# Kernel optimization log

Measured on AMD Instinct MI355X. Metric: run time of the kernel, lower is better.

## Reference

```python
import jax, jax.numpy as jnp
import numpy as np

B, N, D_IN, D, H = 4, 256, 600, 600, 256  # batch, nodes, in_dim, mem_dim, attn hidden


def setup_inputs() -> dict:
    key = jax.random.key(0)
    ks = jax.random.split(key, 12)
    feature = jax.random.normal(ks[0], (B, N, D_IN), dtype=jnp.float32)
    latent_adj = jax.random.randint(ks[1], (B, N, N), 0, 2).astype(jnp.float32)
    s_in = 1.0 / np.sqrt(D_IN)
    s_d = 1.0 / np.sqrt(D)
    s_2d = 1.0 / np.sqrt(2 * D)
    s_h = 1.0 / np.sqrt(H)
    W0 = jax.random.uniform(ks[2], (D_IN, D), jnp.float32, -s_in, s_in)
    b0 = jax.random.uniform(ks[3], (D,), jnp.float32, -s_in, s_in)
    W1 = jax.random.uniform(ks[4], (D, D), jnp.float32, -s_d, s_d)
    b1 = jax.random.uniform(ks[5], (D,), jnp.float32, -s_d, s_d)
    aW1 = jax.random.uniform(ks[6], (2 * D, H), jnp.float32, -s_2d, s_2d)
    ab1 = jax.random.uniform(ks[7], (H,), jnp.float32, -s_2d, s_2d)
    aW2 = jax.random.uniform(ks[8], (H,), jnp.float32, -s_h, s_h)
    ab2 = jax.random.uniform(ks[9], (1,), jnp.float32, -s_h, s_h)
    return {"feature": feature, "latent_adj": latent_adj, "W0": W0, "b0": b0,
            "W1": W1, "b1": b1, "aW1": aW1, "ab1": ab1, "aW2": aW2, "ab2": ab2}


def _gat_layer(x, Wl, bl, aW1, ab1, aW2, ab2, adj):
    h = jnp.einsum('bni,io->bno', x, Wl) + bl                    # [B,N,D]
    # Decompose first attn linear: [h_i, h_j] @ aW1 = h_i @ aW1[:D] + h_j @ aW1[D:]
    left = jnp.einsum('bnd,dh->bnh', h, aW1[:h.shape[-1]])        # i-part
    right = jnp.einsum('bnd,dh->bnh', h, aW1[h.shape[-1]:])       # j-part
    hid = jax.nn.relu(left[:, :, None, :] + right[:, None, :, :] + ab1)  # [B,N,N,H]
    e = jax.nn.leaky_relu(jnp.einsum('bijh,h->bij', hid, aW2) + ab2[0],
                          negative_slope=0.01)                    # [B,N,N]
    e = jnp.where(adj == 0, jnp.float32(-1e9), e)
    attention = jax.nn.softmax(e, axis=-1) * adj
    return jax.nn.relu(jnp.einsum('bij,bjd->bid', attention, h))


def reference(feature, latent_adj, W0, b0, W1, b1, aW1, ab1, aW2, ab2):
    h = _gat_layer(feature, W0, b0, aW1, ab1, aW2, ab2, latent_adj)
    h = _gat_layer(h, W1, b1, aW1, ab1, aW2, ab2, latent_adj)
    return h
```

## Files before the change

### kernel.cpp

```cpp
#include <hip/hip_runtime.h>
#include <hip/hip_bf16.h>

#define BATCH 4
#define NN    256
#define DD    600
#define HH    256
#define MROWS (BATCH*NN)
#define KPAD  640

typedef __attribute__((ext_vector_type(8))) short bf16x8;
typedef __attribute__((ext_vector_type(4))) float f32x4;

__device__ __forceinline__ void gload16(const void* g, void* l)
{
    __builtin_amdgcn_global_load_lds(
        (const __attribute__((address_space(1))) void*)g,
        (__attribute__((address_space(3))) void*)l, 16, 0, 0);
}

__device__ __forceinline__ void waitcnt_vm(int n)
{
    switch (n) {
    case 0:  asm volatile("s_waitcnt vmcnt(0)"  ::: "memory"); break;
    case 4:  asm volatile("s_waitcnt vmcnt(4)"  ::: "memory"); break;
    case 8:  asm volatile("s_waitcnt vmcnt(8)"  ::: "memory"); break;
    case 12: asm volatile("s_waitcnt vmcnt(12)" ::: "memory"); break;
    default: asm volatile("s_waitcnt vmcnt(0)"  ::: "memory"); break;
    }
}

template<bool BIAS, bool RELU, bool WF32, bool WB16, bool WHT, int NK>
__global__ __launch_bounds__(256) void gemm_mfma(
    const __hip_bfloat16* __restrict__ A, const __hip_bfloat16* __restrict__ BT,
    const float* __restrict__ bias,
    float* __restrict__ Cf, __hip_bfloat16* __restrict__ Cb,
    __hip_bfloat16* __restrict__ hT,
    int lda, int ldb, int ldcf, int ldcb, int Nvalid, int biasN,
    long long sA, long long sBT, long long sCf, long long sCb)
{
    __shared__ __align__(16) char lds[65536];

    const int bz   = blockIdx.z;
    const int tid  = threadIdx.x;
    const int lane = tid & 63;
    const int wid  = tid >> 6;
    const int wr   = wid >> 1;
    const int wc   = wid & 1;
    const int row0 = blockIdx.y * 64;
    const int col0 = blockIdx.x * 64;

    const char* Ab = (const char*)A + (bz * sA + (long long)row0 * lda) * 2;
    const char* Bb = (const char*)BT + (bz * sBT + (long long)col0 * ldb) * 2;

    const int sr   = tid >> 3;
    const int scb  = (tid & 7) * 16;
    const int scbs = scb ^ ((sr & 7) << 4);

    const char* gA0 = Ab + (long long)sr        * (lda * 2) + scbs;
    const char* gA1 = Ab + (long long)(sr + 32) * (lda * 2) + scbs;
    const char* gB0 = Bb + (long long)sr        * (ldb * 2) + scbs;
    const char* gB1 = Bb + (long long)(sr + 32) * (ldb * 2) + scbs;

    f32x4 acc[2][2] = {};

    const int fr = lane & 15;
    const int kg = (lane >> 4) * 16;
    const int xv = (fr & 7) << 4;

    auto issue = [&](int t) {
        char* bA = lds + (t & 3) * 8192;
        char* bB = lds + 32768 + (t & 3) * 8192;
        const long long off = (long long)t * 128;
        gload16(gA0 + off, bA + wid * 1024);
        gload16(gA1 + off, bA + 4096 + wid * 1024);
        gload16(gB0 + off, bB + wid * 1024);
        gload16(gB1 + off, bB + 4096 + wid * 1024);
    };

    constexpr int PRE = (NK < 3) ? NK : 3;
    #pragma unroll
    for (int p = 0; p < PRE; ++p) issue(p);

    #pragma unroll
    for (int t = 0; t < NK; ++t) {
        const int imax = (t + 2 < NK - 1) ? t + 2 : NK - 1;
        waitcnt_vm(4 * (imax - t));
        __builtin_amdgcn_s_barrier();
        const char* ldsA = lds + (t & 3) * 8192;
        const char* ldsB = lds + 32768 + (t & 3) * 8192;
        #pragma unroll
        for (int ks = 0; ks < 2; ++ks) {
            const int kb = ks * 64 + kg;
            bf16x8 a0 = *(const bf16x8*)(ldsA + (wr * 32 + fr)      * 128 + (kb ^ xv));
            bf16x8 a1 = *(const bf16x8*)(ldsA + (wr * 32 + 16 + fr) * 128 + (kb ^ xv));
            bf16x8 b0 = *(const bf16x8*)(ldsB + (wc * 32 + fr)      * 128 + (kb ^ xv));
            bf16x8 b1 = *(const bf16x8*)(ldsB + (wc * 32 + 16 + fr) * 128 + (kb ^ xv));
            acc[0][0] = __builtin_amdgcn_mfma_f32_16x16x32_bf16(a0, b0, acc[0][0], 0, 0, 0);
            acc[0][1] = __builtin_amdgcn_mfma_f32_16x16x32_bf16(a0, b1, acc[0][1], 0, 0, 0);
            acc[1][0] = __builtin_amdgcn_mfma_f32_16x16x32_bf16(a1, b0, acc[1][0], 0, 0, 0);
            acc[1][1] = __builtin_amdgcn_mfma_f32_16x16x32_bf16(a1, b1, acc[1][1], 0, 0, 0);
        }
        if (t + 3 < NK) issue(t + 3);
    }
    __syncthreads();

    const int er = (lane >> 4) * 4;
    const int ec = lane & 15;
    __hip_bfloat16* sT = (__hip_bfloat16*)lds;

    #pragma unroll
    for (int mi = 0; mi < 2; ++mi) {
        #pragma unroll
        for (int ni = 0; ni < 2; ++ni) {
            const int lr0 = wr * 32 + mi * 16 + er;
            const int lc  = wc * 32 + ni * 16 + ec;
            const int gr = row0 + lr0;
            const int gc = col0 + lc;
            const float bv = (BIAS && gc < biasN) ? bias[gc] : 0.f;
            #pragma unroll
            for (int r = 0; r < 4; ++r) {
                float v = acc[mi][ni][r] + bv;
                if (RELU) v = fmaxf(v, 0.f);
                const __hip_bfloat16 hv = __float2bfloat16(v);
                const long long row = gr + r;
                if (WF32 && gc < Nvalid)
                    Cf[bz * sCf + row * ldcf + gc] = v;
                if (WB16)
                    Cb[bz * sCb + row * ldcb + gc] = hv;
                if (WHT)
                    sT[(lr0 + r) * 72 + lc] = hv;
            }
        }
    }

    if (WHT) {
        __syncthreads();
        const int b  = row0 >> 8;
        const int i0 = row0 & 255;
        const int cc = tid >> 3;
        const int ch = tid & 7;
        #pragma unroll
        for (int p = 0; p < 2; ++p) {
            const int d = col0 + cc + p * 32;
            __align__(16) __hip_bfloat16 tmp[8];
            #pragma unroll
            for (int u = 0; u < 8; ++u)
                tmp[u] = sT[(ch * 8 + u) * 72 + cc + p * 32];
            *(float4*)&hT[((long long)b * KPAD + d) * NN + i0 + ch * 8] = *(float4*)tmp;
        }
    }
}

__global__ __launch_bounds__(256) void prep_kernel(
    const float* __restrict__ feature, const float* __restrict__ W0,
    const float* __restrict__ W1, const float* __restrict__ aW1,
    __hip_bfloat16* __restrict__ xb, __hip_bfloat16* __restrict__ W0T,
    __hip_bfloat16* __restrict__ W1T, __hip_bfloat16* __restrict__ aW1T)
{
    const int bid = blockIdx.x;
    const int tid = threadIdx.x;
    if (bid < 640) {
        const int idx = (bid * 256 + tid) * 4;
        const int r = idx / KPAD, c = idx % KPAD;
        float4 v = make_float4(0.f, 0.f, 0.f, 0.f);
        if (c < DD) v = *(const float4*)&feature[r * DD + c];
        __align__(8) __hip_bfloat16 o[4] = {
            __float2bfloat16(v.x), __float2bfloat16(v.y),
            __float2bfloat16(v.z), __float2bfloat16(v.w)};
        *(float2*)&xb[idx] = *(float2*)o;
        return;
    }
    __shared__ float tile[32][33];
    const int t = bid - 640;
    const int which = (t < 400) ? 0 : (t < 800) ? 1 : 2;
    const int tt = (which == 0) ? t : (which == 1) ? t - 400 : t - 800;
    const int n0 = (tt / 20) * 32;
    const int k0 = (tt % 20) * 32;
    const int tx = tid & 31, ty = tid >> 5;
    #pragma unroll
    for (int r = 0; r < 4; ++r) {
        const int k = k0 + ty + r * 8;
        const int n = n0 + tx;
        float v = 0.f;
        if (which == 0)      { if (k < DD && n < DD) v = W0[k * DD + n]; }
        else if (which == 1) { if (k < DD && n < DD) v = W1[k * DD + n]; }
        else                 { if (k < DD) v = (n < HH) ? aW1[k * HH + n]
                                                        : aW1[(DD + k) * HH + (n - HH)]; }
        tile[ty + r * 8][tx] = v;
    }
    __syncthreads();
    __hip_bfloat16* dst = (which == 0) ? W0T : (which == 1) ? W1T : aW1T;
    #pragma unroll
    for (int r = 0; r < 4; ++r) {
        const int n = n0 + ty + r * 8;
        const int k = k0 + tx;
        dst[n * KPAD + k] = __float2bfloat16(tile[tx][ty + r * 8]);
    }
}

__device__ __forceinline__ void block_max4(float* v, float (*red)[4])
{
    #pragma unroll
    for (int o = 32; o > 0; o >>= 1)
        #pragma unroll
        for (int q = 0; q < 4; ++q) v[q] = fmaxf(v[q], __shfl_down(v[q], o));
    const int lane = threadIdx.x & 63, w = threadIdx.x >> 6;
    if (lane == 0) { red[w][0]=v[0]; red[w][1]=v[1]; red[w][2]=v[2]; red[w][3]=v[3]; }
    __syncthreads();
    #pragma unroll
    for (int q = 0; q < 4; ++q)
        v[q] = fmaxf(fmaxf(red[0][q], red[1][q]), fmaxf(red[2][q], red[3][q]));
    __syncthreads();
}

__device__ __forceinline__ void block_sum4(float* v, float (*red)[4])
{
    #pragma unroll
    for (int o = 32; o > 0; o >>= 1)
        #pragma unroll
        for (int q = 0; q < 4; ++q) v[q] += __shfl_down(v[q], o);
    const int lane = threadIdx.x & 63, w = threadIdx.x >> 6;
    if (lane == 0) { red[w][0]=v[0]; red[w][1]=v[1]; red[w][2]=v[2]; red[w][3]=v[3]; }
    __syncthreads();
    #pragma unroll
    for (int q = 0; q < 4; ++q)
        v[q] = red[0][q] + red[1][q] + red[2][q] + red[3][q];
    __syncthreads();
}

__global__ __launch_bounds__(256) void attn_kernel(
    const float* __restrict__ LR, const float* __restrict__ aW2,
    const float* __restrict__ ab2, const float* __restrict__ adj,
    __hip_bfloat16* __restrict__ att)
{
    __shared__ float sL[4][HH];
    __shared__ float sW[HH];
    __shared__ float red[4][4];

    const int b  = blockIdx.y;
    const int i0 = blockIdx.x * 4;
    const int j  = threadIdx.x;

    sW[j] = aW2[j];
    #pragma unroll
    for (int q = 0; q < 4; ++q)
        sL[q][j] = LR[((long long)(b * NN + i0 + q)) * 512 + j];
    __syncthreads();

    const float* rp = LR + ((long long)(b * NN + j)) * 512 + HH;
    float acc[4] = {0.f, 0.f, 0.f, 0.f};
    for (int h = 0; h < HH; h += 8) {
        const float4 ra = *(const float4*)(rp + h);
        const float4 rb = *(const float4*)(rp + h + 4);
        const float4 w0 = *(const float4*)&sW[h];
        const float4 w1 = *(const float4*)&sW[h + 4];
        #pragma unroll
        for (int q = 0; q < 4; ++q) {
            const float4 l0 = *(const float4*)&sL[q][h];
            const float4 l1 = *(const float4*)&sL[q][h + 4];
            float s = fmaxf(l0.x + ra.x, 0.f) * w0.x;
            s += fmaxf(l0.y + ra.y, 0.f) * w0.y;
            s += fmaxf(l0.z + ra.z, 0.f) * w0.z;
            s += fmaxf(l0.w + ra.w, 0.f) * w0.w;
            s += fmaxf(l1.x + rb.x, 0.f) * w1.x;
            s += fmaxf(l1.y + rb.y, 0.f) * w1.y;
            s += fmaxf(l1.z + rb.z, 0.f) * w1.z;
            s += fmaxf(l1.w + rb.w, 0.f) * w1.w;
            acc[q] += s;
        }
    }

    const float ab2v = ab2[0];
    float m[4], a[4];
    #pragma unroll
    for (int q = 0; q < 4; ++q) {
        float e = acc[q] + ab2v;
        e = (e > 0.f) ? e : 0.01f * e;
        a[q] = adj[((long long)(b * NN + i0 + q)) * NN + j];
        m[q] = (a[q] == 0.f) ? -1e9f : e;
    }
    float mx[4] = {m[0], m[1], m[2], m[3]};
    block_max4(mx, red);
    float p[4];
    #pragma unroll
    for (int q = 0; q < 4; ++q) p[q] = __expf(m[q] - mx[q]);
    float s[4] = {p[0], p[1], p[2], p[3]};
    block_sum4(s, red);
    #pragma unroll
    for (int q = 0; q < 4; ++q)
        att[((long long)(b * NN + i0 + q)) * NN + j] = __float2bfloat16(p[q] / s[q] * a[q]);
}

extern "C" void kernel_launch(void* const* d_in, const int* in_sizes, int n_in,
                              void* d_out, int out_size, void* d_ws, size_t ws_size,
                              hipStream_t stream)
{
    const float* feature = (const float*)d_in[0];
    const float* adj     = (const float*)d_in[1];
    const float* W0      = (const float*)d_in[2];
    const float* b0      = (const float*)d_in[3];
    const float* W1      = (const float*)d_in[4];
    const float* b1      = (const float*)d_in[5];
    const float* aW1     = (const float*)d_in[6];
    const float* ab1     = (const float*)d_in[7];
    const float* aW2     = (const float*)d_in[8];
    const float* ab2     = (const float*)d_in[9];
    float* out = (float*)d_out;

    __hip_bfloat16* bw = (__hip_bfloat16*)d_ws;
    __hip_bfloat16* xb   = bw;
    __hip_bfloat16* W0T  = xb   + MROWS * KPAD;
    __hip_bfloat16* W1T  = W0T  + KPAD * KPAD;
    __hip_bfloat16* aW1T = W1T  + KPAD * KPAD;
    __hip_bfloat16* hb   = aW1T + 512 * KPAD;
    __hip_bfloat16* hT   = hb   + MROWS * KPAD;
    __hip_bfloat16* att  = hT   + BATCH * KPAD * NN;
    float* LR = (float*)(att + BATCH * NN * NN);

    prep_kernel<<<1760, 256, 0, stream>>>(feature, W0, W1, aW1, xb, W0T, W1T, aW1T);

    for (int layer = 0; layer < 2; ++layer) {
        const __hip_bfloat16* WT = layer ? W1T : W0T;
        const float* bb          = layer ? b1 : b0;

        gemm_mfma<true, false, false, true, true, KPAD/64><<<dim3(KPAD / 64, MROWS / 64, 1), 256, 0, stream>>>(
            xb, WT, bb, nullptr, hb, hT,
            KPAD, KPAD, 0, KPAD, 0, DD, 0, 0, 0, 0);

        gemm_mfma<true, false, true, false, false, KPAD/64><<<dim3(512 / 64, MROWS / 64, 1), 256, 0, stream>>>(
            hb, aW1T, ab1, LR, nullptr, nullptr,
            KPAD, KPAD, 512, 0, 512, HH, 0, 0, 0, 0);

        attn_kernel<<<dim3(NN / 4, BATCH), 256, 0, stream>>>(LR, aW2, ab2, adj, att);

        if (layer == 0) {
            gemm_mfma<false, true, false, true, false, NN/64><<<dim3(KPAD / 64, NN / 64, BATCH), 256, 0, stream>>>(
                att, hT, nullptr, nullptr, xb, nullptr,
                NN, NN, 0, KPAD, 0, 0,
                (long long)NN * NN, (long long)KPAD * NN, 0, (long long)NN * KPAD);
        } else {
            gemm_mfma<false, true, true, false, false, NN/64><<<dim3(KPAD / 64, NN / 64, BATCH), 256, 0, stream>>>(
                att, hT, nullptr, out, nullptr, nullptr,
                NN, NN, DD, 0, DD, 0,
                (long long)NN * NN, (long long)KPAD * NN, (long long)NN * DD, 0);
        }
    }
}
```

Before: 68.51 us.

## Fold attention projection into node linear via precomputed W·aW1 combined weight

Precomputes W_l·aW1 (left and right halves) in the prep kernel and stacks it with W_l into one 1152-column weight, with a matching fused bias. Each layer then runs a single GEMM that produces h (bf16 plus its transpose) and the left/right attention projections (fp32) together. This removes one GEMM launch per layer and its serial dependency on h. In exchange the prep kernel does an extra small matmul, and the projections are computed from the composed bf16 weights rather than from bf16-rounded h, which changes rounding slightly.

```diff
diff --git a/kernel.cpp b/kernel.cpp
--- a/kernel.cpp
+++ b/kernel.cpp
@@ -7,6 +7,7 @@
 #define HH    256
 #define MROWS (BATCH*NN)
 #define KPAD  640
+#define NFUSE 1152
 
 typedef __attribute__((ext_vector_type(8))) short bf16x8;
 typedef __attribute__((ext_vector_type(4))) float f32x4;
@@ -29,7 +30,7 @@
     }
 }
 
-template<bool BIAS, bool RELU, bool WF32, bool WB16, bool WHT, int NK>
+template<bool BIAS, bool RELU, bool WF32, bool WB16, bool WHT, int NK, bool FUSEDLR>
 __global__ __launch_bounds__(256) void gemm_mfma(
     const __hip_bfloat16* __restrict__ A, const __hip_bfloat16* __restrict__ BT,
     const float* __restrict__ bias,
@@ -108,6 +109,7 @@
     const int ec = lane & 15;
     __hip_bfloat16* sT = (__hip_bfloat16*)lds;
 
+    const bool doBias = BIAS && (col0 < biasN);
     #pragma unroll
     for (int mi = 0; mi < 2; ++mi) {
         #pragma unroll
@@ -116,24 +118,33 @@
             const int lc  = wc * 32 + ni * 16 + ec;
             const int gr = row0 + lr0;
             const int gc = col0 + lc;
-            const float bv = (BIAS && gc < biasN) ? bias[gc] : 0.f;
+            const float bv = doBias ? bias[gc] : 0.f;
             #pragma unroll
             for (int r = 0; r < 4; ++r) {
                 float v = acc[mi][ni][r] + bv;
                 if (RELU) v = fmaxf(v, 0.f);
                 const __hip_bfloat16 hv = __float2bfloat16(v);
                 const long long row = gr + r;
-                if (WF32 && gc < Nvalid)
-                    Cf[bz * sCf + row * ldcf + gc] = v;
-                if (WB16)
-                    Cb[bz * sCb + row * ldcb + gc] = hv;
-                if (WHT)
-                    sT[(lr0 + r) * 72 + lc] = hv;
+                if (FUSEDLR) {
+                    if (gc < KPAD) {
+                        Cb[row * ldcb + gc] = hv;
+                        sT[(lr0 + r) * 72 + lc] = hv;
+                    } else {
+                        Cf[row * ldcf + (gc - KPAD)] = v;
+                    }
+                } else {
+                    if (WF32 && gc < Nvalid)
+                        Cf[bz * sCf + row * ldcf + gc] = v;
+                    if (WB16)
+                        Cb[bz * sCb + row * ldcb + gc] = hv;
+                    if (WHT)
+                        sT[(lr0 + r) * 72 + lc] = hv;
+                }
             }
         }
     }
 
-    if (WHT) {
+    if (WHT && (!FUSEDLR || col0 < KPAD)) {
         __syncthreads();
         const int b  = row0 >> 8;
         const int i0 = row0 & 255;
@@ -154,13 +165,110 @@
 __global__ __launch_bounds__(256) void prep_kernel(
     const float* __restrict__ feature, const float* __restrict__ W0,
     const float* __restrict__ W1, const float* __restrict__ aW1,
-    __hip_bfloat16* __restrict__ xb, __hip_bfloat16* __restrict__ W0T,
-    __hip_bfloat16* __restrict__ W1T, __hip_bfloat16* __restrict__ aW1T)
-{
-    const int bid = blockIdx.x;
+    const float* __restrict__ b0, const float* __restrict__ b1,
+    const float* __restrict__ ab1,
+    __hip_bfloat16* __restrict__ xb, __hip_bfloat16* __restrict__ UT0,
+    __hip_bfloat16* __restrict__ UT1, float* __restrict__ fb0,
+    float* __restrict__ fb1)
+{
+    __shared__ __align__(16) char smem[18432];
+    const int u   = blockIdx.x;
     const int tid = threadIdx.x;
-    if (bid < 640) {
-        const int idx = (bid * 256 + tid) * 4;
+
+    if (u < 160) {
+        const int l  = u / 80;
+        const int t  = u % 80;
+        const int n0 = (t / 10) * 64;
+        const int i0 = (t % 10) * 64;
+        const int p  = n0 >> 8;
+        const int nH0 = n0 & 255;
+        const float* Wl = l ? W1 : W0;
+        __hip_bfloat16* UT = l ? UT1 : UT0;
+
+        __hip_bfloat16* At = (__hip_bfloat16*)smem;
+        __hip_bfloat16* Bt = At + 64 * 72;
+
+        const int lane = tid & 63, wid = tid >> 6;
+        const int wr = wid >> 1, wc = wid & 1;
+        const int fr = lane & 15;
+        const int k8 = (lane >> 4) * 8;
+
+        f32x4 acc[2][2] = {};
+
+        for (int d0 = 0; d0 < 640; d0 += 64) {
+            __syncthreads();
+            #pragma unroll
+            for (int P = 0; P < 4; ++P) {
+                const int d  = d0 + (tid >> 4) + P * 16;
+                const int n4 = (tid & 15) * 4;
+                float4 v = make_float4(0.f, 0.f, 0.f, 0.f);
+                if (d < 600) v = *(const float4*)&aW1[(long long)(d + 600 * p) * 256 + nH0 + n4];
+                const float* vf = (const float*)&v;
+                #pragma unroll
+                for (int j2 = 0; j2 < 4; ++j2)
+                    At[(n4 + j2) * 72 + (d - d0)] = __float2bfloat16(vf[j2]);
+            }
+            #pragma unroll
+            for (int P = 0; P < 4; ++P) {
+                const int li = (tid >> 4) + P * 16;
+                const int d4 = (tid & 15) * 4;
+                float4 v = make_float4(0.f, 0.f, 0.f, 0.f);
+                if (d0 + d4 < 600) v = *(const float4*)&Wl[(long long)(i0 + li) * 600 + d0 + d4];
+                __align__(8) __hip_bfloat16 o[4] = {
+                    __float2bfloat16(v.x), __float2bfloat16(v.y),
+                    __float2bfloat16(v.z), __float2bfloat16(v.w)};
+                *(float2*)&Bt[li * 72 + d4] = *(float2*)o;
+            }
+            __syncthreads();
+            #pragma unroll
+            for (int ks = 0; ks < 2; ++ks) {
+                const int kb = ks * 32 + k8;
+                bf16x8 a0 = *(const bf16x8*)&At[(wr * 32 + fr)      * 72 + kb];
+                bf16x8 a1 = *(const bf16x8*)&At[(wr * 32 + 16 + fr) * 72 + kb];
+                bf16x8 b0r = *(const bf16x8*)&Bt[(wc * 32 + fr)      * 72 + kb];
+                bf16x8 b1r = *(const bf16x8*)&Bt[(wc * 32 + 16 + fr) * 72 + kb];
+                acc[0][0] = __builtin_amdgcn_mfma_f32_16x16x32_bf16(a0, b0r, acc[0][0], 0, 0, 0);
+                acc[0][1] = __builtin_amdgcn_mfma_f32_16x16x32_bf16(a0, b1r, acc[0][1], 0, 0, 0);
+                acc[1][0] = __builtin_amdgcn_mfma_f32_16x16x32_bf16(a1, b0r, acc[1][0], 0, 0, 0);
+                acc[1][1] = __builtin_amdgcn_mfma_f32_16x16x32_bf16(a1, b1r, acc[1][1], 0, 0, 0);
+            }
+        }
+        const int er = (lane >> 4) * 4;
+        const int ec = lane & 15;
+        #pragma unroll
+        for (int mi = 0; mi < 2; ++mi)
+            #pragma unroll
+            for (int ni = 0; ni < 2; ++ni) {
+                const int rr = n0 + wr * 32 + mi * 16 + er;
+                const int cc = i0 + wc * 32 + ni * 16 + ec;
+                #pragma unroll
+                for (int r = 0; r < 4; ++r)
+                    UT[(long long)(640 + rr + r) * 640 + cc] =
+                        __float2bfloat16(acc[mi][ni][r]);
+            }
+        return;
+    }
+    if (u < 164) {
+        const int idx = u - 160;
+        const int l = idx >> 1, p = idx & 1;
+        const float* bl = l ? b1 : b0;
+        float* fb = l ? fb1 : fb0;
+        float acc = 0.f;
+        for (int d = 0; d < 600; ++d)
+            acc += bl[d] * aW1[(long long)(d + 600 * p) * 256 + tid];
+        fb[640 + p * 256 + tid] = acc + (p == 0 ? ab1[tid] : 0.f);
+        return;
+    }
+    if (u < 169) {
+        const int e = (u - 164) * 256 + tid;
+        const int l = e / 640, c = e % 640;
+        float* fb = l ? fb1 : fb0;
+        const float* bl = l ? b1 : b0;
+        fb[c] = (c < 600) ? bl[c] : 0.f;
+        return;
+    }
+    if (u < 809) {
+        const int idx = ((u - 169) * 256 + tid) * 4;
         const int r = idx / KPAD, c = idx % KPAD;
         float4 v = make_float4(0.f, 0.f, 0.f, 0.f);
         if (c < DD) v = *(const float4*)&feature[r * DD + c];
@@ -170,26 +278,24 @@
         *(float2*)&xb[idx] = *(float2*)o;
         return;
     }
-    __shared__ float tile[32][33];
-    const int t = bid - 640;
-    const int which = (t < 400) ? 0 : (t < 800) ? 1 : 2;
-    const int tt = (which == 0) ? t : (which == 1) ? t - 400 : t - 800;
+    float (*tile)[33] = (float(*)[33])smem;
+    const int t = u - 809;
+    const int which = (t < 400) ? 0 : 1;
+    const int tt = which ? t - 400 : t;
     const int n0 = (tt / 20) * 32;
     const int k0 = (tt % 20) * 32;
     const int tx = tid & 31, ty = tid >> 5;
+    const float* Wl = which ? W1 : W0;
     #pragma unroll
     for (int r = 0; r < 4; ++r) {
         const int k = k0 + ty + r * 8;
         const int n = n0 + tx;
         float v = 0.f;
-        if (which == 0)      { if (k < DD && n < DD) v = W0[k * DD + n]; }
-        else if (which == 1) { if (k < DD && n < DD) v = W1[k * DD + n]; }
-        else                 { if (k < DD) v = (n < HH) ? aW1[k * HH + n]
-                                                        : aW1[(DD + k) * HH + (n - HH)]; }
+        if (k < DD && n < DD) v = Wl[k * DD + n];
         tile[ty + r * 8][tx] = v;
     }
     __syncthreads();
-    __hip_bfloat16* dst = (which == 0) ? W0T : (which == 1) ? W1T : aW1T;
+    __hip_bfloat16* dst = which ? UT1 : UT0;
     #pragma unroll
     for (int r = 0; r < 4; ++r) {
         const int n = n0 + ty + r * 8;
@@ -309,37 +415,38 @@
 
     __hip_bfloat16* bw = (__hip_bfloat16*)d_ws;
     __hip_bfloat16* xb   = bw;
-    __hip_bfloat16* W0T  = xb   + MROWS * KPAD;
-    __hip_bfloat16* W1T  = W0T  + KPAD * KPAD;
-    __hip_bfloat16* aW1T = W1T  + KPAD * KPAD;
-    __hip_bfloat16* hb   = aW1T + 512 * KPAD;
-    __hip_bfloat16* hT   = hb   + MROWS * KPAD;
-    __hip_bfloat16* att  = hT   + BATCH * KPAD * NN;
-    float* LR = (float*)(att + BATCH * NN * NN);
-
-    prep_kernel<<<1760, 256, 0, stream>>>(feature, W0, W1, aW1, xb, W0T, W1T, aW1T);
+    __hip_bfloat16* UT0  = xb  + MROWS * KPAD;
+    __hip_bfloat16* UT1  = UT0 + NFUSE * KPAD;
+    __hip_bfloat16* hb   = UT1 + NFUSE * KPAD;
+    __hip_bfloat16* hT   = hb  + MROWS * KPAD;
+    __hip_bfloat16* att  = hT  + BATCH * KPAD * NN;
+    float* LR  = (float*)(att + BATCH * NN * NN);
+    float* fb0 = LR + MROWS * 512;
+    float* fb1 = fb0 + NFUSE;
+
+    prep_kernel<<<1609, 256, 0, stream>>>(
+        feature, W0, W1, aW1, b0, b1, ab1, xb, UT0, UT1, fb0, fb1);
 
     for (int layer = 0; layer < 2; ++layer) {
-        const __hip_bfloat16* WT = layer ? W1T : W0T;
-        const float* bb          = layer ? b1 : b0;
-
-        gemm_mfma<true, false, false, true, true, KPAD/64><<<dim3(KPAD / 64, MROWS / 64, 1), 256, 0, stream>>>(
-            xb, WT, bb, nullptr, hb, hT,
-            KPAD, KPAD, 0, KPAD, 0, DD, 0, 0, 0, 0);
-
-        gemm_mfma<true, false, true, false, false, KPAD/64><<<dim3(512 / 64, MROWS / 64, 1), 256, 0, stream>>>(
-            hb, aW1T, ab1, LR, nullptr, nullptr,
-            KPAD, KPAD, 512, 0, 512, HH, 0, 0, 0, 0);
+        const __hip_bfloat16* UT = layer ? UT1 : UT0;
+        const float* fb          = layer ? fb1 : fb0;
+
+        gemm_mfma<true, false, true, true, true, KPAD/64, true>
+            <<<dim3(NFUSE / 64, MROWS / 64, 1), 256, 0, stream>>>(
+            xb, UT, fb, LR, hb, hT,
+            KPAD, KPAD, 512, KPAD, 0, NFUSE, 0, 0, 0, 0);
 
         attn_kernel<<<dim3(NN / 4, BATCH), 256, 0, stream>>>(LR, aW2, ab2, adj, att);
 
         if (layer == 0) {
-            gemm_mfma<false, true, false, true, false, NN/64><<<dim3(KPAD / 64, NN / 64, BATCH), 256, 0, stream>>>(
+            gemm_mfma<false, true, false, true, false, NN/64, false>
+                <<<dim3(KPAD / 64, NN / 64, BATCH), 256, 0, stream>>>(
                 att, hT, nullptr, nullptr, xb, nullptr,
                 NN, NN, 0, KPAD, 0, 0,
                 (long long)NN * NN, (long long)KPAD * NN, 0, (long long)NN * KPAD);
         } else {
-            gemm_mfma<false, true, true, false, false, NN/64><<<dim3(KPAD / 64, NN / 64, BATCH), 256, 0, stream>>>(
+            gemm_mfma<false, true, true, false, false, NN/64, false>
+                <<<dim3(KPAD / 64, NN / 64, BATCH), 256, 0, stream>>>(
                 att, hT, nullptr, out, nullptr, nullptr,
                 NN, NN, DD, 0, DD, 0,
                 (long long)NN * NN, (long long)KPAD * NN, (long long)NN * DD, 0);
```

Measured after the change: 82.71 us. 20.7% more time.
